# Performance work log

Hardware: AMD Instinct MI355X
Metric: run time of the kernel (lower is better)

Reference implementation:

```python
import jax, jax.numpy as jnp
import numpy as np

# Model hyperparameters (match init_kwargs)
D, N, M_DIM, L, BATCH = 10, 500, 5, 6, 1024
W_STD, B_STD, A_STD = 0.1, 0.0, 1.0


def softplus10(x):
    return jax.nn.softplus(10.0 * x) / 10.0


def setup_inputs() -> dict:
    key = jax.random.key(0)
    ks = jax.random.split(key, 7)
    w_scale = W_STD / np.sqrt(M_DIM).astype(np.float32)
    return {
        "X": jax.random.normal(ks[0], (BATCH, D), dtype=jnp.float32),
        "w_first": W_STD * jax.random.normal(ks[1], (D, N, 1, M_DIM), dtype=jnp.float32),
        "w_mid": w_scale * jax.random.normal(ks[2], (L - 2, D, N, M_DIM, M_DIM), dtype=jnp.float32),
        "w_last": w_scale * jax.random.normal(ks[3], (D, N, M_DIM, 1), dtype=jnp.float32),
        "bs": B_STD * jax.random.normal(ks[4], (L - 1, D, N, M_DIM), dtype=jnp.float32),
        "b_last": B_STD * jax.random.normal(ks[5], (D, N, 1), dtype=jnp.float32),
        "a_all": A_STD * jax.random.normal(ks[6], (L - 1, D, N, M_DIM), dtype=jnp.float32),
    }


def reference(X, w_first, w_mid, w_last, bs, b_last, a_all):
    # X: [M, d] -> phis: [M, d, n, 1]
    Mb = X.shape[0]
    phis = jnp.broadcast_to(X[:, :, None, None], (Mb, D, N, 1))
    phidots = jnp.ones_like(phis)  # [M, d, n, 1]

    ws = [w_first] + [w_mid[i] for i in range(L - 2)]
    for l in range(L - 1):
        W = softplus10(ws[l])                                    # [d,n,k,m]
        pre = jnp.einsum('mjik,jikl->mjil', phis, W) + bs[l]     # [M,d,n,m]
        ta = jnp.tanh(a_all[l])                                  # [d,n,m]
        tanhdot = 1.0 - jnp.tanh(pre) ** 2                       # tanh'(pre)
        phidots = jnp.einsum('mjik,jikl->mjil', phidots, W) * (1.0 + ta * tanhdot)
        phis = pre + jnp.tanh(pre) * ta

    Wl = softplus10(w_last)                                      # [d,n,m,1]
    pre = jnp.einsum('mjik,jikl->mjil', phis, Wl) + b_last       # [M,d,n,1]
    s = jax.nn.sigmoid(pre)
    phidots = jnp.einsum('mjik,jikl->mjil', phidots, Wl) * (s * (1.0 - s))

    fm = jax.lax.stop_gradient(-jnp.log(phidots + 1e-10))        # [M,d,n,1]
    fm = jnp.min(jnp.mean(fm, axis=1, keepdims=True), axis=2, keepdims=True)
    return jnp.squeeze(phidots, -1), fm.reshape(-1)              # ([M,d,n], [M])
```

## Files before the change

### kernel.cpp

```cpp
#include <hip/hip_runtime.h>
#include <math.h>

#define D_ 10
#define N_ 500
#define REC 164

typedef float f32x2 __attribute__((ext_vector_type(2)));

__device__ __forceinline__ float fexp2(float x){ return __builtin_amdgcn_exp2f(x); }
__device__ __forceinline__ float flog2(float x){ return __builtin_amdgcn_logf(x); }
__device__ __forceinline__ float frcp (float x){ return __builtin_amdgcn_rcpf(x); }

#define LOG2E 1.4426950408889634f
#define LN2   0.6931471805599453f

__device__ __forceinline__ float fast_tanh(float x){
  float e = fexp2(x * (2.0f*LOG2E));
  return 1.0f - 2.0f*frcp(e + 1.0f);
}
__device__ __forceinline__ float softplus10(float x){
  float e = fexp2(x * (10.0f*LOG2E));
  return (0.1f*LN2) * flog2(1.0f + e);
}

__device__ __forceinline__ void act_tanh(f32x2 pre, f32x2* th, f32x2* td){
  f32x2 e;
  e.x = fexp2(pre.x * (2.0f*LOG2E));
  e.y = fexp2(pre.y * (2.0f*LOG2E));
  f32x2 p1 = e + 1.0f;
  float pr = p1.x * p1.y;
  float rr = frcp(pr);
  f32x2 rc;
  rc.x = p1.y * rr;
  rc.y = p1.x * rr;
  f32x2 t = 1.0f - 2.0f*rc;
  *th = t;
  *td = 1.0f - t*t;
}

__global__ __launch_bounds__(256) void tennet_prep(
    const float* __restrict__ w_first, const float* __restrict__ w_mid,
    const float* __restrict__ w_last, const float* __restrict__ bs,
    const float* __restrict__ b_last, const float* __restrict__ a_all,
    float* __restrict__ rec)
{
  int rid = blockIdx.x*4 + (threadIdx.x >> 6);
  int lane = threadIdx.x & 63;
  int d = rid / N_;
  int n = rid - d*N_;
  float* dst = rec + rid*REC;
  for (int i = lane; i < 161; i += 64) {
    float v;
    if (i < 5)        v = softplus10(w_first[(d*N_+n)*5 + i]);
    else if (i < 10)  v = bs[(d*N_+n)*5 + (i-5)];
    else if (i < 15)  v = fast_tanh(a_all[(d*N_+n)*5 + (i-10)]);
    else if (i < 155) {
      int q = i - 15; int l = q/35; int r2 = q - l*35;
      if (r2 < 25) {
        int j = r2/5, k = r2 - (r2/5)*5;
        v = softplus10(w_mid[((l*D_+d)*N_+n)*25 + k*5 + j]);
      } else if (r2 < 30) {
        v = bs[(((l+1)*D_+d)*N_+n)*5 + (r2-25)];
      } else {
        v = fast_tanh(a_all[(((l+1)*D_+d)*N_+n)*5 + (r2-30)]);
      }
    }
    else if (i < 160) v = softplus10(w_last[(d*N_+n)*5 + (i-155)]);
    else              v = b_last[d*N_+n];
    dst[i] = v;
  }
}

__global__ __launch_bounds__(512) void tennet_main(
    const float* __restrict__ X, const float* __restrict__ rec,
    float* __restrict__ out0)
{
  __shared__ float tr[128*9];
  int bid = blockIdx.x;
  int mb  = bid & 7;
  int q   = bid >> 3;
  int d   = q / 63;
  int nch = q - d*63;
  int n0 = nch*8;
  int t = threadIdx.x;
  int wv = __builtin_amdgcn_readfirstlane(t >> 6);
  int lane = t & 63;
  int n = n0 + wv;
  int nr = (n < N_) ? n : (N_-1);
  const float* r = rec + (d*N_ + nr)*REC;
  int m0 = mb*128 + lane;

  f32x2 x;
  x.x = X[m0*D_ + d];
  x.y = X[(m0+64)*D_ + d];

  f32x2 phis[5], phid[5];
  #pragma unroll
  for (int j = 0; j < 5; ++j) {
    f32x2 pre = x * r[j] + r[5+j];
    f32x2 th, td;
    act_tanh(pre, &th, &td);
    phid[j] = (1.0f + r[10+j]*td) * r[j];
    phis[j] = pre + th * r[10+j];
  }
  #pragma unroll
  for (int l = 0; l < 4; ++l) {
    const int base = 15 + l*35;
    f32x2 nphis[5], nphid[5];
    #pragma unroll
    for (int j = 0; j < 5; ++j) {
      f32x2 pre = phis[0] * r[base + j*5] + r[base + 25 + j];
      f32x2 pd  = phid[0] * r[base + j*5];
      #pragma unroll
      for (int k = 1; k < 5; ++k) {
        pre += phis[k] * r[base + j*5 + k];
        pd  += phid[k] * r[base + j*5 + k];
      }
      f32x2 th, td;
      act_tanh(pre, &th, &td);
      nphid[j] = pd * (1.0f + r[base + 30 + j]*td);
      nphis[j] = pre + th * r[base + 30 + j];
    }
    #pragma unroll
    for (int j = 0; j < 5; ++j){ phis[j]=nphis[j]; phid[j]=nphid[j]; }
  }
  f32x2 pre = phis[0] * r[155] + r[160];
  f32x2 pd  = phid[0] * r[155];
  #pragma unroll
  for (int k = 1; k < 5; ++k) {
    pre += phis[k] * r[155 + k];
    pd  += phid[k] * r[155 + k];
  }
  f32x2 e;
  e.x = fexp2(pre.x * (-LOG2E));
  e.y = fexp2(pre.y * (-LOG2E));
  f32x2 p1 = e + 1.0f;
  float prd = p1.x * p1.y;
  float rrc = frcp(prd);
  f32x2 sg;
  sg.x = p1.y * rrc;
  sg.y = p1.x * rrc;
  f32x2 res = pd * sg * (1.0f - sg);

  tr[lane*9 + wv]      = res.x;
  tr[(lane+64)*9 + wv] = res.y;
  __syncthreads();
  int tn = t & 7;
  #pragma unroll
  for (int p = 0; p < 2; ++p) {
    int rr2 = (t >> 3) + p*64;
    if (n0 + tn < N_)
      out0[((mb*128 + rr2)*D_ + d)*N_ + n0 + tn] = tr[rr2*9 + tn];
  }
}

__global__ __launch_bounds__(512) void tennet_fm(
    const float* __restrict__ out0, float* __restrict__ fm)
{
  int m = blockIdx.x;
  int t = threadIdx.x;
  float val = INFINITY;
  if (t < N_) {
    float acc = 0.0f;
    #pragma unroll
    for (int d = 0; d < D_; ++d) {
      float v = out0[(m*D_ + d)*N_ + t];
      acc += flog2(v + 1e-10f);
    }
    val = -acc * (LN2 / (float)D_);
  }
  #pragma unroll
  for (int off = 32; off; off >>= 1) {
    float o = __shfl_down(val, off, 64);
    val = fminf(val, o);
  }
  __shared__ float red[8];
  int wid = t >> 6;
  if ((t & 63) == 0) red[wid] = val;
  __syncthreads();
  if (t == 0) {
    float v = red[0];
    #pragma unroll
    for (int ww = 1; ww < 8; ++ww) v = fminf(v, red[ww]);
    fm[m] = v;
  }
}

extern "C" void kernel_launch(void* const* d_in, const int* in_sizes, int n_in,
                              void* d_out, int out_size, void* d_ws, size_t ws_size,
                              hipStream_t stream) {
  const float* X       = (const float*)d_in[0];
  const float* w_first = (const float*)d_in[1];
  const float* w_mid   = (const float*)d_in[2];
  const float* w_last  = (const float*)d_in[3];
  const float* bs      = (const float*)d_in[4];
  const float* b_last  = (const float*)d_in[5];
  const float* a_all   = (const float*)d_in[6];
  float* out0 = (float*)d_out;
  float* fm   = out0 + 1024*D_*N_;
  float* rec  = (float*)d_ws;

  tennet_prep<<<(D_*N_)/4, 256, 0, stream>>>(w_first, w_mid, w_last, bs, b_last, a_all, rec);
  tennet_main<<<10*63*8, 512, 0, stream>>>(X, rec, out0);
  tennet_fm<<<1024, 512, 0, stream>>>(out0, fm);
}
```

Baseline: 66.05 us.

## Switch per-neuron parameters and layer math to packed fp16 FMA

Parameters are stored as fp16 in a padded 184-entry record, and the per-neuron MLP runs in packed fp16. v_pk_fma_f16 reads the weights as scalar operands through op_sel, and tanh/sigmoid are still evaluated in fp32. The aim is to halve parameter bandwidth and scalar loads and double ALU throughput per instruction. In exchange, precision drops, and phidots accumulated over six layers in fp16 may fail tolerance or underflow ahead of the log in fm.

```diff
diff --git a/kernel.cpp b/kernel.cpp
--- a/kernel.cpp
+++ b/kernel.cpp
@@ -3,14 +3,19 @@
 
 #define D_ 10
 #define N_ 500
-#define REC 164
+#define REC_H 184
 
 typedef float f32x2 __attribute__((ext_vector_type(2)));
+typedef _Float16 h2 __attribute__((ext_vector_type(2)));
 
 __device__ __forceinline__ float fexp2(float x){ return __builtin_amdgcn_exp2f(x); }
 __device__ __forceinline__ float flog2(float x){ return __builtin_amdgcn_logf(x); }
 __device__ __forceinline__ float frcp (float x){ return __builtin_amdgcn_rcpf(x); }
 
+__device__ __forceinline__ h2 cvt_pk(float a, float b){
+  return __builtin_bit_cast(h2, __builtin_amdgcn_cvt_pkrtz(a, b));
+}
+
 #define LOG2E 1.4426950408889634f
 #define LN2   0.6931471805599453f
 
@@ -23,56 +28,77 @@
   return (0.1f*LN2) * flog2(1.0f + e);
 }
 
-__device__ __forceinline__ void act_tanh(f32x2 pre, f32x2* th, f32x2* td){
-  f32x2 e;
-  e.x = fexp2(pre.x * (2.0f*LOG2E));
-  e.y = fexp2(pre.y * (2.0f*LOG2E));
-  f32x2 p1 = e + 1.0f;
-  float pr = p1.x * p1.y;
-  float rr = frcp(pr);
-  f32x2 rc;
-  rc.x = p1.y * rr;
-  rc.y = p1.x * rr;
-  f32x2 t = 1.0f - 2.0f*rc;
+__device__ __forceinline__ h2 pkh_fma_blo(h2 a, unsigned w, h2 c){
+  h2 d; asm("v_pk_fma_f16 %0, %1, %2, %3 op_sel:[0,0,0] op_sel_hi:[1,0,1]"
+            : "=v"(d) : "v"(a), "s"(w), "v"(c)); return d; }
+__device__ __forceinline__ h2 pkh_fma_bhi(h2 a, unsigned w, h2 c){
+  h2 d; asm("v_pk_fma_f16 %0, %1, %2, %3 op_sel:[0,1,0] op_sel_hi:[1,1,1]"
+            : "=v"(d) : "v"(a), "s"(w), "v"(c)); return d; }
+__device__ __forceinline__ h2 pkh_mul_blo(h2 a, unsigned w){
+  h2 d; asm("v_pk_mul_f16 %0, %1, %2 op_sel:[0,0] op_sel_hi:[1,0]"
+            : "=v"(d) : "v"(a), "s"(w)); return d; }
+__device__ __forceinline__ h2 pkh_mul_bhi(h2 a, unsigned w){
+  h2 d; asm("v_pk_mul_f16 %0, %1, %2 op_sel:[0,1] op_sel_hi:[1,1]"
+            : "=v"(d) : "v"(a), "s"(w)); return d; }
+__device__ __forceinline__ h2 pkh_mul(h2 a, h2 b){
+  h2 d; asm("v_pk_mul_f16 %0, %1, %2" : "=v"(d) : "v"(a), "v"(b)); return d; }
+__device__ __forceinline__ h2 pkh_nfma(h2 a, h2 b, h2 c){
+  h2 d; asm("v_pk_fma_f16 %0, %1, %2, %3 neg_lo:[1,0,0] neg_hi:[1,0,0]"
+            : "=v"(d) : "v"(a), "v"(b), "v"(c)); return d; }
+
+#define LDW(hh)          (*(const unsigned*)(rw16 + ((hh) & ~1)))
+#define FMH_B(a, hh, c)  (((hh)&1) ? pkh_fma_bhi((a), LDW(hh), (c)) : pkh_fma_blo((a), LDW(hh), (c)))
+#define MUH_B(a, hh)     (((hh)&1) ? pkh_mul_bhi((a), LDW(hh))      : pkh_mul_blo((a), LDW(hh)))
+
+__device__ __forceinline__ void act_tanh(h2 pre, h2 ONEH, h2* th, h2* td){
+  float p0 = (float)pre.x, p1 = (float)pre.y;
+  float e0 = fexp2(p0 * (2.0f*LOG2E));
+  float e1 = fexp2(p1 * (2.0f*LOG2E));
+  float q0 = e0 + 1.0f, q1 = e1 + 1.0f;
+  float rr = frcp(q0 * q1);
+  float t0 = 1.0f - 2.0f*(q1*rr);
+  float t1 = 1.0f - 2.0f*(q0*rr);
+  h2 t = cvt_pk(t0, t1);
   *th = t;
-  *td = 1.0f - t*t;
+  *td = pkh_nfma(t, t, ONEH);
 }
 
 __global__ __launch_bounds__(256) void tennet_prep(
     const float* __restrict__ w_first, const float* __restrict__ w_mid,
     const float* __restrict__ w_last, const float* __restrict__ bs,
     const float* __restrict__ b_last, const float* __restrict__ a_all,
-    float* __restrict__ rec)
+    unsigned short* __restrict__ rec16)
 {
   int rid = blockIdx.x*4 + (threadIdx.x >> 6);
   int lane = threadIdx.x & 63;
   int d = rid / N_;
   int n = rid - d*N_;
-  float* dst = rec + rid*REC;
-  for (int i = lane; i < 161; i += 64) {
-    float v;
+  unsigned short* dst = rec16 + (unsigned)rid*REC_H;
+  for (int i = lane; i < REC_H; i += 64) {
+    float v = 0.0f;
     if (i < 5)        v = softplus10(w_first[(d*N_+n)*5 + i]);
     else if (i < 10)  v = bs[(d*N_+n)*5 + (i-5)];
     else if (i < 15)  v = fast_tanh(a_all[(d*N_+n)*5 + (i-10)]);
-    else if (i < 155) {
-      int q = i - 15; int l = q/35; int r2 = q - l*35;
+    else if (i < 175) {
+      int q = i - 15; int l = q/40; int r2 = q - l*40;
       if (r2 < 25) {
         int j = r2/5, k = r2 - (r2/5)*5;
         v = softplus10(w_mid[((l*D_+d)*N_+n)*25 + k*5 + j]);
       } else if (r2 < 30) {
         v = bs[(((l+1)*D_+d)*N_+n)*5 + (r2-25)];
-      } else {
+      } else if (r2 < 35) {
         v = fast_tanh(a_all[(((l+1)*D_+d)*N_+n)*5 + (r2-30)]);
       }
     }
-    else if (i < 160) v = softplus10(w_last[(d*N_+n)*5 + (i-155)]);
-    else              v = b_last[d*N_+n];
-    dst[i] = v;
+    else if (i < 180) v = softplus10(w_last[(d*N_+n)*5 + (i-175)]);
+    else if (i == 180) v = b_last[d*N_+n];
+    _Float16 hv = (_Float16)v;
+    dst[i] = __builtin_bit_cast(unsigned short, hv);
   }
 }
 
 __global__ __launch_bounds__(512) void tennet_main(
-    const float* __restrict__ X, const float* __restrict__ rec,
+    const float* __restrict__ X, const unsigned short* __restrict__ rec16,
     float* __restrict__ out0)
 {
   __shared__ float tr[128*9];
@@ -87,63 +113,68 @@
   int lane = t & 63;
   int n = n0 + wv;
   int nr = (n < N_) ? n : (N_-1);
-  const float* r = rec + (d*N_ + nr)*REC;
+  const unsigned short* rw16 = rec16 + (unsigned)(d*N_ + nr)*REC_H;
   int m0 = mb*128 + lane;
 
-  f32x2 x;
-  x.x = X[m0*D_ + d];
-  x.y = X[(m0+64)*D_ + d];
-
-  f32x2 phis[5], phid[5];
+  float xa = X[m0*D_ + d];
+  float xb = X[(m0+64)*D_ + d];
+  h2 x = cvt_pk(xa, xb);
+
+  h2 ONEH; ONEH.x = (_Float16)1.0f; ONEH.y = (_Float16)1.0f;
+
+  h2 phis[5], phid[5];
   #pragma unroll
   for (int j = 0; j < 5; ++j) {
-    f32x2 pre = x * r[j] + r[5+j];
-    f32x2 th, td;
-    act_tanh(pre, &th, &td);
-    phid[j] = (1.0f + r[10+j]*td) * r[j];
-    phis[j] = pre + th * r[10+j];
+    h2 bias = MUH_B(ONEH, 5+j);
+    h2 pre = FMH_B(x, j, bias);
+    h2 th, td;
+    act_tanh(pre, ONEH, &th, &td);
+    h2 uf = FMH_B(td, 10+j, ONEH);
+    phid[j] = MUH_B(uf, j);
+    phis[j] = FMH_B(th, 10+j, pre);
   }
   #pragma unroll
   for (int l = 0; l < 4; ++l) {
-    const int base = 15 + l*35;
-    f32x2 nphis[5], nphid[5];
+    const int B = 15 + l*40;
+    h2 nphis[5], nphid[5];
     #pragma unroll
     for (int j = 0; j < 5; ++j) {
-      f32x2 pre = phis[0] * r[base + j*5] + r[base + 25 + j];
-      f32x2 pd  = phid[0] * r[base + j*5];
+      h2 bias = MUH_B(ONEH, B + 25 + j);
+      h2 pre = FMH_B(phis[0], B + j*5, bias);
+      h2 pd  = MUH_B(phid[0], B + j*5);
       #pragma unroll
       for (int k = 1; k < 5; ++k) {
-        pre += phis[k] * r[base + j*5 + k];
-        pd  += phid[k] * r[base + j*5 + k];
+        pre = FMH_B(phis[k], B + j*5 + k, pre);
+        pd  = FMH_B(phid[k], B + j*5 + k, pd);
       }
-      f32x2 th, td;
-      act_tanh(pre, &th, &td);
-      nphid[j] = pd * (1.0f + r[base + 30 + j]*td);
-      nphis[j] = pre + th * r[base + 30 + j];
+      h2 th, td;
+      act_tanh(pre, ONEH, &th, &td);
+      h2 uf = FMH_B(td, B + 30 + j, ONEH);
+      nphid[j] = pkh_mul(pd, uf);
+      nphis[j] = FMH_B(th, B + 30 + j, pre);
     }
     #pragma unroll
     for (int j = 0; j < 5; ++j){ phis[j]=nphis[j]; phid[j]=nphid[j]; }
   }
-  f32x2 pre = phis[0] * r[155] + r[160];
-  f32x2 pd  = phid[0] * r[155];
+  h2 biasl = MUH_B(ONEH, 180);
+  h2 preh = FMH_B(phis[0], 175, biasl);
+  h2 pdh  = MUH_B(phid[0], 175);
   #pragma unroll
   for (int k = 1; k < 5; ++k) {
-    pre += phis[k] * r[155 + k];
-    pd  += phid[k] * r[155 + k];
-  }
-  f32x2 e;
-  e.x = fexp2(pre.x * (-LOG2E));
-  e.y = fexp2(pre.y * (-LOG2E));
-  f32x2 p1 = e + 1.0f;
-  float prd = p1.x * p1.y;
-  float rrc = frcp(prd);
-  f32x2 sg;
-  sg.x = p1.y * rrc;
-  sg.y = p1.x * rrc;
-  f32x2 res = pd * sg * (1.0f - sg);
-
-  tr[lane*9 + wv]      = res.x;
-  tr[(lane+64)*9 + wv] = res.y;
+    preh = FMH_B(phis[k], 175 + k, preh);
+    pdh  = FMH_B(phid[k], 175 + k, pdh);
+  }
+  float z0 = (float)preh.x, z1 = (float)preh.y;
+  float e0 = fexp2(z0 * (-LOG2E));
+  float e1 = fexp2(z1 * (-LOG2E));
+  float q0 = e0 + 1.0f, q1 = e1 + 1.0f;
+  float rr = frcp(q0 * q1);
+  float s0 = q1*rr, s1 = q0*rr;
+  float res0 = (float)pdh.x * s0 * (1.0f - s0);
+  float res1 = (float)pdh.y * s1 * (1.0f - s1);
+
+  tr[lane*9 + wv]      = res0;
+  tr[(lane+64)*9 + wv] = res1;
   __syncthreads();
   int tn = t & 7;
   #pragma unroll
@@ -198,9 +229,9 @@
   const float* a_all   = (const float*)d_in[6];
   float* out0 = (float*)d_out;
   float* fm   = out0 + 1024*D_*N_;
-  float* rec  = (float*)d_ws;
-
-  tennet_prep<<<(D_*N_)/4, 256, 0, stream>>>(w_first, w_mid, w_last, bs, b_last, a_all, rec);
-  tennet_main<<<10*63*8, 512, 0, stream>>>(X, rec, out0);
+  unsigned short* rec16 = (unsigned short*)d_ws;
+
+  tennet_prep<<<(D_*N_)/4, 256, 0, stream>>>(w_first, w_mid, w_last, bs, b_last, a_all, rec16);
+  tennet_main<<<10*63*8, 512, 0, stream>>>(X, rec16, out0);
   tennet_fm<<<1024, 512, 0, stream>>>(out0, fm);
 }
```

Measured after the change: 76.50 us. +15.8%, slower.
